# Kernel tuning notes

Measured on AMD Instinct MI355X. Metric: run time of the kernel, lower is better.

## Reference

```python
import math
import jax, jax.numpy as jnp
import numpy as np

N_HEADS = 8
FACTOR = 1.0


def setup_inputs() -> dict:
    key = jax.random.key(0)
    ks = jax.random.split(key, 5)
    B, L, D = 8, 4096, 512
    scale = 0.02
    def w(k):
        return jax.random.normal(k, (D, D), jnp.float32) * scale
    return {
        "hidden_states": jax.random.normal(ks[0], (B, L, D), jnp.float32),
        "Wq": w(ks[1]), "bq": jnp.zeros((D,), jnp.float32),
        "Wk": w(ks[2]), "bk": jnp.zeros((D,), jnp.float32),
        "Wv": w(ks[3]), "bv": jnp.zeros((D,), jnp.float32),
        "Wo": w(ks[4]), "bo": jnp.zeros((D,), jnp.float32),
    }


def reference(hidden_states, Wq, bq, Wk, bk, Wv, bv, Wo, bo):
    B, L, D = hidden_states.shape
    H = N_HEADS
    Hd = D // H

    def proj(W, b):
        y = hidden_states @ W.T + b                      # [B, L, D]
        return y.reshape(B, L, H, Hd).transpose(0, 2, 3, 1)  # [B, H, Hd, L]

    q = proj(Wq, bq)
    k = proj(Wk, bk)
    v = proj(Wv, bv)

    # period-based auto-correlation via FFT: corr(tau) = sum_t q(t) k(t - tau)
    qf = jnp.fft.rfft(q, axis=-1)
    kf = jnp.fft.rfft(k, axis=-1)
    corr = jnp.fft.irfft(qf * jnp.conj(kf), n=L, axis=-1)   # [B, H, Hd, L]

    # time-delay aggregation (eval branch): per-batch top-k delays
    mean_corr = corr.mean(axis=(1, 2))                      # [B, L]
    top_k = int(FACTOR * math.log(L))
    weights, delays = jax.lax.top_k(mean_corr, top_k)       # [B, k]
    weights = jax.nn.softmax(weights, axis=-1)

    # circular gather: pattern[b,h,d,i,l] = v[b,h,d,(l + delay[b,i]) % L]
    idx = (jnp.arange(L)[None, None, :] + delays[:, :, None]) % L  # [B, k, L]
    gathered = jax.vmap(lambda vb, ib: vb[:, :, ib])(v, idx)       # [B, H, Hd, k, L]
    agg = jnp.einsum("bhdkl,bk->bhdl", gathered, weights)          # [B, H, Hd, L]

    ctx = agg.transpose(0, 3, 1, 2).reshape(B, L, D)        # [B, L, D]
    return ctx @ Wo.T + bo
```

## Files before the change

kernel.cpp:

```cpp
#include <hip/hip_runtime.h>
#include <math.h>

#define NB 8
#define NL 4096
#define ND 512
#define NK 8

typedef unsigned short ushort_t;
typedef __bf16 bf16x8 __attribute__((ext_vector_type(8)));
typedef float f32x4 __attribute__((ext_vector_type(4)));

__device__ __forceinline__ unsigned short f2bf(float x) {
    unsigned u = __builtin_bit_cast(unsigned, x);
    u += 0x7fff + ((u >> 16) & 1);
    return (unsigned short)(u >> 16);
}
__device__ __forceinline__ float bf2f(unsigned short b) {
    unsigned u = ((unsigned)b) << 16;
    return __builtin_bit_cast(float, u);
}

__global__ void k_smallgemm(const float* __restrict__ A, const float* __restrict__ Bm,
                            float* __restrict__ C, int sa_k, int sa_i, int sb_k, int sb_j) {
    int i = blockIdx.y * 16 + threadIdx.y;
    int j = blockIdx.x * 16 + threadIdx.x;
    float acc = 0.f;
    for (int k = 0; k < ND; ++k)
        acc += A[k * sa_k + i * sa_i] * Bm[k * sb_k + j * sb_j];
    C[i * ND + j] = acc;
}

__global__ void k_biasprep(const float* __restrict__ Wo, const float* __restrict__ bv,
                           const float* __restrict__ bo, float* __restrict__ bp) {
    int i = blockIdx.x * blockDim.x + threadIdx.x;
    float acc = bo[i];
    for (int k = 0; k < ND; ++k) acc += Wo[i * ND + k] * bv[k];
    bp[i] = acc;
}

__global__ __launch_bounds__(256) void k_split(const float* __restrict__ src,
                                               ushort_t* __restrict__ dst) {
    int gid = blockIdx.x * 256 + threadIdx.x;
    int row = gid >> 7;
    int kc = (gid & 127) * 4;
    float4 v = *(const float4*)(src + (size_t)row * ND + kc);
    ushort4 hi, lo;
    hi.x = f2bf(v.x); lo.x = f2bf(v.x - bf2f(hi.x));
    hi.y = f2bf(v.y); lo.y = f2bf(v.y - bf2f(hi.y));
    hi.z = f2bf(v.z); lo.z = f2bf(v.z - bf2f(hi.z));
    hi.w = f2bf(v.w); lo.w = f2bf(v.w - bf2f(hi.w));
    *(ushort4*)(dst + (size_t)row * 1024 + kc) = hi;
    *(ushort4*)(dst + (size_t)row * 1024 + 512 + kc) = lo;
}

__global__ __launch_bounds__(256) void k_transpose(const float* __restrict__ X,
                                                   float* __restrict__ XT) {
    __shared__ float t[32][33];
    int b  = blockIdx.z;
    int l0 = blockIdx.x * 32;
    int c0 = blockIdx.y * 32;
    const float* Xb = X + (size_t)b * NL * ND;
    float* XTb = XT + (size_t)b * ND * NL;
    int tx = threadIdx.x, ty = threadIdx.y;
#pragma unroll
    for (int j = 0; j < 4; ++j)
        t[ty + j * 8][tx] = Xb[(size_t)(l0 + ty + j * 8) * ND + c0 + tx];
    __syncthreads();
#pragma unroll
    for (int j = 0; j < 4; ++j)
        XTb[(size_t)(c0 + ty + j * 8) * NL + l0 + tx] = t[tx][ty + j * 8];
}

template <int EPI>
__global__ __launch_bounds__(512, 2) void k_gemm_split(const ushort_t* __restrict__ As,
                                                       const ushort_t* __restrict__ Bs,
                                                       const float* __restrict__ bp,
                                                       float* __restrict__ Out) {
    struct Buf { ushort_t ahi[256 * 32]; ushort_t alo[256 * 32];
                 ushort_t bhi[256 * 32]; ushort_t blo[256 * 32]; };
    __shared__ union USm {
        Buf s[2];
        float t[32 * 257];
    } sm;
    const int tid = threadIdx.x;
    const int flat = blockIdx.x + (blockIdx.y << 7);
    const int wswz = ((flat & 7) << 5) + (flat >> 3);
    const int l0 = (wswz >> 1) * 256;
    const int n0 = (wswz & 1) * 256;
    const int lane = tid & 63;
    const int w = tid >> 6;
    const int wr = (w & 1) * 128;
    const int wc = (w >> 1) * 64;
    const int m = lane & 15;
    const int quad = lane >> 4;

    f32x4 acc[8][4];
#pragma unroll
    for (int i = 0; i < 8; ++i)
#pragma unroll
        for (int j = 0; j < 4; ++j) acc[i][j] = (f32x4){0.f, 0.f, 0.f, 0.f};

    auto STAGE = [&](int bf, int k0) {
#pragma unroll
        for (int v = 0; v < 2; ++v) {
            int q = v * 512 + tid;
            int row = ((q >> 6) << 4) | (q & 15);
            int kc = (q >> 4) & 3;
            const ushort_t* asrc = As + (size_t)(l0 + row) * 1024 + k0 + kc * 8;
            __builtin_amdgcn_global_load_lds(
                (const __attribute__((address_space(1))) unsigned int*)asrc,
                (__attribute__((address_space(3))) unsigned int*)&sm.s[bf].ahi[q * 8], 16, 0, 0);
            __builtin_amdgcn_global_load_lds(
                (const __attribute__((address_space(1))) unsigned int*)(asrc + 512),
                (__attribute__((address_space(3))) unsigned int*)&sm.s[bf].alo[q * 8], 16, 0, 0);
            const ushort_t* bsrc = Bs + (size_t)(n0 + row) * 1024 + k0 + kc * 8;
            __builtin_amdgcn_global_load_lds(
                (const __attribute__((address_space(1))) unsigned int*)bsrc,
                (__attribute__((address_space(3))) unsigned int*)&sm.s[bf].bhi[q * 8], 16, 0, 0);
            __builtin_amdgcn_global_load_lds(
                (const __attribute__((address_space(1))) unsigned int*)(bsrc + 512),
                (__attribute__((address_space(3))) unsigned int*)&sm.s[bf].blo[q * 8], 16, 0, 0);
        }
    };

    auto COMPUTE = [&](int bf) {
        bf16x8 ah[8], al[8];
#pragma unroll
        for (int i = 0; i < 8; ++i) {
            int off = ((wr >> 4) + i) * 512 + lane * 8;
            ah[i] = *(const bf16x8*)&sm.s[bf].ahi[off];
            al[i] = *(const bf16x8*)&sm.s[bf].alo[off];
        }
        __builtin_amdgcn_s_setprio(1);
#pragma unroll
        for (int j = 0; j < 4; ++j) {
            int off = ((wc >> 4) + j) * 512 + lane * 8;
            bf16x8 bh = *(const bf16x8*)&sm.s[bf].bhi[off];
            bf16x8 bl = *(const bf16x8*)&sm.s[bf].blo[off];
#pragma unroll
            for (int i = 0; i < 8; ++i) {
                acc[i][j] = __builtin_amdgcn_mfma_f32_16x16x32_bf16(ah[i], bh, acc[i][j], 0, 0, 0);
                acc[i][j] = __builtin_amdgcn_mfma_f32_16x16x32_bf16(ah[i], bl, acc[i][j], 0, 0, 0);
                acc[i][j] = __builtin_amdgcn_mfma_f32_16x16x32_bf16(al[i], bh, acc[i][j], 0, 0, 0);
            }
        }
        __builtin_amdgcn_s_setprio(0);
    };

    STAGE(0, 0);
    STAGE(1, 32);
    for (int t = 0; t < 15; ++t) {
        asm volatile("s_waitcnt vmcnt(8)" ::: "memory");
        __builtin_amdgcn_sched_barrier(0);
        __builtin_amdgcn_s_barrier();
        COMPUTE(t & 1);
        asm volatile("s_waitcnt lgkmcnt(0)" ::: "memory");
        __builtin_amdgcn_sched_barrier(0);
        __builtin_amdgcn_s_barrier();
        __builtin_amdgcn_sched_barrier(0);
        if (t < 14) STAGE(t & 1, (t + 2) * 32);
    }
    asm volatile("s_waitcnt vmcnt(0)" ::: "memory");
    __builtin_amdgcn_sched_barrier(0);
    __builtin_amdgcn_s_barrier();
    COMPUTE(1);

    if (EPI == 1) {
#pragma unroll
        for (int j = 0; j < 4; ++j) {
            int col = n0 + wc + 16 * j + m;
            float bv = bp[col];
#pragma unroll
            for (int i = 0; i < 8; ++i) {
                size_t rbase = (size_t)(l0 + wr + 16 * i + quad * 4) * ND + col;
#pragma unroll
                for (int r = 0; r < 4; ++r)
                    Out[rbase + (size_t)r * ND] = acc[i][j][r] + bv;
            }
        }
    } else {
#pragma unroll
        for (int c = 0; c < 8; ++c) {
            __syncthreads();
            if ((wc >> 6) == (c >> 1)) {
                int jb = (c & 1) * 2;
#pragma unroll
                for (int jj = 0; jj < 2; ++jj) {
                    int j = jb + jj;
                    int cl = 16 * jj + m;
#pragma unroll
                    for (int i = 0; i < 8; ++i)
#pragma unroll
                        for (int r = 0; r < 4; ++r)
                            sm.t[cl * 257 + wr + 16 * i + quad * 4 + r] = acc[i][j][r];
                }
            }
            __syncthreads();
#pragma unroll
            for (int it = 0; it < 16; ++it) {
                int idx = it * 512 + tid;
                int cl = idx >> 8;
                int row = idx & 255;
                int rg = l0 + row;
                Out[((size_t)((rg >> 12) * ND + n0 + c * 32 + cl)) * NL + (rg & 4095)] =
                    sm.t[cl * 257 + row];
            }
        }
    }
}

template <int DIR>
__device__ __forceinline__ void fft16(float2* v) {
    const float ct[8] = {1.f, 0.923879533f, 0.707106781f, 0.382683432f,
                         0.f, -0.382683432f, -0.707106781f, -0.923879533f};
    const float st[8] = {0.f, 0.382683432f, 0.707106781f, 0.923879533f,
                         1.f, 0.923879533f, 0.707106781f, 0.382683432f};
    const int br[16] = {0, 8, 4, 12, 2, 10, 6, 14, 1, 9, 5, 13, 3, 11, 7, 15};
    float2 a[16];
#pragma unroll
    for (int i = 0; i < 16; ++i) a[i] = v[br[i]];
#pragma unroll
    for (int s = 1; s <= 4; ++s) {
        const int L = 1 << s, h = L >> 1;
#pragma unroll
        for (int g = 0; g < 16; g += L)
#pragma unroll
            for (int p = 0; p < h; ++p) {
                int k = p << (4 - s);
                float wr = ct[k];
                float wi = (DIR > 0) ? -st[k] : st[k];
                int i1 = g + p, i2 = i1 + h;
                float tr = wr * a[i2].x - wi * a[i2].y;
                float ti = wr * a[i2].y + wi * a[i2].x;
                a[i2].x = a[i1].x - tr; a[i2].y = a[i1].y - ti;
                a[i1].x += tr;          a[i1].y += ti;
            }
    }
#pragma unroll
    for (int i = 0; i < 16; ++i) v[i] = a[i];
}

__device__ __forceinline__ float2 cmul(float2 a, float2 b) {
    return make_float2(a.x * b.x - a.y * b.y, a.x * b.y + a.y * b.x);
}
#define PADI(i) ((i) + ((i) >> 4))

__global__ __launch_bounds__(256) void k_fft_fwd(const float* __restrict__ XT,
                                                 const float* __restrict__ YT,
                                                 float2* __restrict__ partial) {
    __shared__ float2 data[4352];
    const int t = threadIdx.x;
    const int b = blockIdx.x >> 6;
    const int g = blockIdx.x & 63;

    float sv, cv;
    sincosf(-6.283185307179586f * (float)(t & 15) / 256.0f, &sv, &cv);
    const float2 w2 = make_float2(cv, sv);
    sincosf(-6.283185307179586f * (float)t / 4096.0f, &sv, &cv);
    const float2 w3 = make_float2(cv, sv);

    float2 acc[16];
#pragma unroll
    for (int r = 0; r < 16; ++r) acc[r] = make_float2(0.f, 0.f);

    for (int ch = 0; ch < 8; ++ch) {
        int c = g * 8 + ch;
        const float* xr = XT + ((size_t)b * ND + c) * NL;
        const float* yr = YT + ((size_t)b * ND + c) * NL;
        float2 v[16];
#pragma unroll
        for (int mm = 0; mm < 16; ++mm)
            v[mm] = make_float2(xr[t + 256 * mm], yr[t + 256 * mm]);
        fft16<1>(v);
        __syncthreads();
#pragma unroll
        for (int mm = 0; mm < 16; ++mm) data[PADI(16 * t + mm)] = v[mm];
        __syncthreads();
#pragma unroll
        for (int mm = 0; mm < 16; ++mm) v[mm] = data[PADI(t + 256 * mm)];
        {
            float2 wm = make_float2(1.f, 0.f);
#pragma unroll
            for (int mm = 1; mm < 16; ++mm) { wm = cmul(wm, w2); v[mm] = cmul(v[mm], wm); }
        }
        fft16<1>(v);
        __syncthreads();
        {
            int base = (t >> 4) * 256 + (t & 15);
#pragma unroll
            for (int mm = 0; mm < 16; ++mm) data[PADI(base + 16 * mm)] = v[mm];
        }
        __syncthreads();
#pragma unroll
        for (int mm = 0; mm < 16; ++mm) v[mm] = data[PADI(t + 256 * mm)];
        {
            float2 wm = make_float2(1.f, 0.f);
#pragma unroll
            for (int mm = 1; mm < 16; ++mm) { wm = cmul(wm, w3); v[mm] = cmul(v[mm], wm); }
        }
        fft16<1>(v);
        __syncthreads();
#pragma unroll
        for (int mm = 0; mm < 16; ++mm) data[PADI(t + 256 * mm)] = v[mm];
        __syncthreads();
#pragma unroll
        for (int mm = 0; mm < 16; ++mm) {
            int f = t + 256 * mm;
            float2 A = v[mm];
            float2 Bz = data[PADI((4096 - f) & 4095)];
            acc[mm].x += 0.5f * (A.x * Bz.y + A.y * Bz.x);
            acc[mm].y += 0.25f * ((A.x * A.x + A.y * A.y) - (Bz.x * Bz.x + Bz.y * Bz.y));
        }
    }
    float2* out = partial + ((size_t)b * 64 + g) * 4096;
#pragma unroll
    for (int mm = 0; mm < 16; ++mm) out[256 * mm + t] = acc[mm];
}

__global__ __launch_bounds__(256) void k_reduce(const float2* __restrict__ partial,
                                                float2* __restrict__ Cf) {
    int b = blockIdx.x >> 4;
    int f = (blockIdx.x & 15) * 256 + threadIdx.x;
    float2 s = make_float2(0.f, 0.f);
    for (int g = 0; g < 64; ++g) {
        float2 v = partial[((size_t)(b * 64 + g)) * 4096 + f];
        s.x += v.x; s.y += v.y;
    }
    Cf[(size_t)b * 4096 + f] = s;
}

__global__ __launch_bounds__(256) void k_ifft(const float2* __restrict__ Cf,
                                              float* __restrict__ mc) {
    __shared__ float2 data[4352];
    const int t = threadIdx.x;
    const int b = blockIdx.x;
    float sv, cv;
    sincosf(6.283185307179586f * (float)(t & 15) / 256.0f, &sv, &cv);
    const float2 w2 = make_float2(cv, sv);
    sincosf(6.283185307179586f * (float)t / 4096.0f, &sv, &cv);
    const float2 w3 = make_float2(cv, sv);

    float2 v[16];
#pragma unroll
    for (int mm = 0; mm < 16; ++mm) v[mm] = Cf[(size_t)b * 4096 + t + 256 * mm];
    fft16<-1>(v);
#pragma unroll
    for (int mm = 0; mm < 16; ++mm) data[PADI(16 * t + mm)] = v[mm];
    __syncthreads();
#pragma unroll
    for (int mm = 0; mm < 16; ++mm) v[mm] = data[PADI(t + 256 * mm)];
    {
        float2 wm = make_float2(1.f, 0.f);
#pragma unroll
        for (int mm = 1; mm < 16; ++mm) { wm = cmul(wm, w2); v[mm] = cmul(v[mm], wm); }
    }
    fft16<-1>(v);
    __syncthreads();
    {
        int base = (t >> 4) * 256 + (t & 15);
#pragma unroll
        for (int mm = 0; mm < 16; ++mm) data[PADI(base + 16 * mm)] = v[mm];
    }
    __syncthreads();
#pragma unroll
    for (int mm = 0; mm < 16; ++mm) v[mm] = data[PADI(t + 256 * mm)];
    {
        float2 wm = make_float2(1.f, 0.f);
#pragma unroll
        for (int mm = 1; mm < 16; ++mm) { wm = cmul(wm, w3); v[mm] = cmul(v[mm], wm); }
    }
    fft16<-1>(v);
    const float scale = 1.0f / (4096.0f * 512.0f);
#pragma unroll
    for (int mm = 0; mm < 16; ++mm)
        mc[(size_t)b * NL + t + 256 * mm] = v[mm].x * scale;
}

__global__ __launch_bounds__(256) void k_topk(const float* __restrict__ mc,
                                              float* __restrict__ wts,
                                              int* __restrict__ dly) {
    __shared__ float vals[4096];
    __shared__ float rv[256];
    __shared__ int ri[256];
    __shared__ float tv[NK];
    __shared__ int tix[NK];
    const int tid = threadIdx.x;
    const int b = blockIdx.x;
    for (int t = tid; t < 4096; t += 256) vals[t] = mc[(size_t)b * NL + t];
    __syncthreads();
    for (int it = 0; it < NK; ++it) {
        float bv = -3.0e38f;
        int bi = 0;
        for (int t = tid; t < 4096; t += 256) {
            float v = vals[t];
            if (v > bv) { bv = v; bi = t; }
        }
        rv[tid] = bv;
        ri[tid] = bi;
        __syncthreads();
        for (int off = 128; off > 0; off >>= 1) {
            if (tid < off) {
                if (rv[tid + off] > rv[tid]) {
                    rv[tid] = rv[tid + off];
                    ri[tid] = ri[tid + off];
                }
            }
            __syncthreads();
        }
        if (tid == 0) {
            tv[it] = rv[0];
            tix[it] = ri[0];
            vals[ri[0]] = -3.0e38f;
        }
        __syncthreads();
    }
    if (tid == 0) {
        float mx = tv[0];
        float e[NK], s = 0.f;
        for (int i = 0; i < NK; ++i) { e[i] = expf(tv[i] - mx); s += e[i]; }
        for (int i = 0; i < NK; ++i) {
            wts[b * NK + i] = e[i] / s;
            dly[b * NK + i] = tix[i];
        }
    }
}

__global__ __launch_bounds__(256) void k_gather(const float* __restrict__ X,
                                                const float* __restrict__ wts,
                                                const int* __restrict__ dly,
                                                ushort_t* __restrict__ Xaggs) {
    __shared__ float sw[NK];
    __shared__ int sd[NK];
    int gid = blockIdx.x * 256 + threadIdx.x;
    int b = gid >> 19;
    int rem = gid & 524287;
    int l = rem >> 7;
    int c4 = rem & 127;
    if (threadIdx.x < NK) {
        sw[threadIdx.x] = wts[b * NK + threadIdx.x];
        sd[threadIdx.x] = dly[b * NK + threadIdx.x];
    }
    __syncthreads();
    const float4* Xb = (const float4*)X + (size_t)b * 524288;
    float4 s = make_float4(0.f, 0.f, 0.f, 0.f);
#pragma unroll
    for (int i = 0; i < NK; ++i) {
        int ls = (l + sd[i]) & (NL - 1);
        float4 v = Xb[(size_t)ls * 128 + c4];
        float w = sw[i];
        s.x += w * v.x;
        s.y += w * v.y;
        s.z += w * v.z;
        s.w += w * v.w;
    }
    ushort4 hi, lo;
    hi.x = f2bf(s.x); lo.x = f2bf(s.x - bf2f(hi.x));
    hi.y = f2bf(s.y); lo.y = f2bf(s.y - bf2f(hi.y));
    hi.z = f2bf(s.z); lo.z = f2bf(s.z - bf2f(hi.z));
    hi.w = f2bf(s.w); lo.w = f2bf(s.w - bf2f(hi.w));
    ushort_t* rowp = Xaggs + (size_t)(b * NL + l) * 1024;
    *(ushort4*)(rowp + c4 * 4) = hi;
    *(ushort4*)(rowp + 512 + c4 * 4) = lo;
}

extern "C" void kernel_launch(void* const* d_in, const int* in_sizes, int n_in,
                              void* d_out, int out_size, void* d_ws, size_t ws_size,
                              hipStream_t stream) {
    (void)in_sizes; (void)n_in; (void)out_size; (void)ws_size;
    const float* X  = (const float*)d_in[0];
    const float* Wq = (const float*)d_in[1];
    const float* Wk = (const float*)d_in[3];
    const float* Wv = (const float*)d_in[5];
    const float* bv = (const float*)d_in[6];
    const float* Wo = (const float*)d_in[7];
    const float* bo = (const float*)d_in[8];
    float* Out = (float*)d_out;

    char* ws = (char*)d_ws;
    const size_t MB = 1024 * 1024;
    float*    M     = (float*)(ws + 0 * MB);
    float*    Wov   = (float*)(ws + 1 * MB);
    ushort_t* BsM   = (ushort_t*)(ws + 2 * MB);
    ushort_t* BsW   = (ushort_t*)(ws + 3 * MB);
    float*    bp    = (float*)(ws + 4 * MB);
    float*    mc    = (float*)(ws + 4 * MB + 0x10000);
    float*    wts   = (float*)(ws + 4 * MB + 0x40000);
    int*      dly   = (int*)(ws + 4 * MB + 0x41000);
    float2*   Cf    = (float2*)(ws + 4 * MB + 0x80000);
    float2*   partial = (float2*)(ws + 5 * MB);
    ushort_t* Xs    = (ushort_t*)(ws + 21 * MB);
    float*    XT    = (float*)(ws + 21 * MB);
    float*    YT    = (float*)(ws + 85 * MB);
    ushort_t* Xaggs = (ushort_t*)(ws + 85 * MB);

    k_smallgemm<<<dim3(32, 32), dim3(16, 16), 0, stream>>>(Wq, Wk, M, ND, 1, ND, 1);
    k_smallgemm<<<dim3(32, 32), dim3(16, 16), 0, stream>>>(Wo, Wv, Wov, 1, ND, ND, 1);
    k_biasprep<<<1, 512, 0, stream>>>(Wo, bv, bo, bp);
    k_split<<<256, 256, 0, stream>>>(M, BsM);
    k_split<<<256, 256, 0, stream>>>(Wov, BsW);

    k_split<<<16384, 256, 0, stream>>>(X, Xs);
    k_gemm_split<0><<<dim3(128, 2), 512, 0, stream>>>(Xs, BsM, nullptr, YT);

    k_transpose<<<dim3(128, 16, NB), dim3(32, 8), 0, stream>>>(X, XT);

    k_fft_fwd<<<512, 256, 0, stream>>>(XT, YT, partial);
    k_reduce<<<128, 256, 0, stream>>>(partial, Cf);
    k_ifft<<<NB, 256, 0, stream>>>(Cf, mc);

    k_topk<<<NB, 256, 0, stream>>>(mc, wts, dly);

    k_gather<<<16384, 256, 0, stream>>>(X, wts, dly, Xaggs);

    k_gemm_split<1><<<dim3(128, 2), 512, 0, stream>>>(Xaggs, BsW, bp, Out);
}
```

Before: 598.2 us.

## Swizzle GEMM LDS tile layout and fuse inverse FFT with top-k

The GEMM staging now stores A and B tiles row-major in LDS with an XOR swizzle on the 8-element column chunk, and the MFMA fragment reads use the matching swizzled offsets. The goal is fewer LDS bank conflicts and more contiguous global reads per row. Separately, the inverse FFT kernel now writes its mean-correlation output straight into shared memory and runs top-k and softmax in the same block. This drops one launch and a global round trip, at the cost of more shared memory per block.

```diff
diff --git a/kernel.cpp b/kernel.cpp
--- a/kernel.cpp
+++ b/kernel.cpp
@@ -104,16 +104,16 @@
 #pragma unroll
         for (int v = 0; v < 2; ++v) {
             int q = v * 512 + tid;
-            int row = ((q >> 6) << 4) | (q & 15);
-            int kc = (q >> 4) & 3;
-            const ushort_t* asrc = As + (size_t)(l0 + row) * 1024 + k0 + kc * 8;
+            int r = q >> 2;
+            int c = (q & 3) ^ ((r >> 1) & 3);
+            const ushort_t* asrc = As + (size_t)(l0 + r) * 1024 + k0 + c * 8;
             __builtin_amdgcn_global_load_lds(
                 (const __attribute__((address_space(1))) unsigned int*)asrc,
                 (__attribute__((address_space(3))) unsigned int*)&sm.s[bf].ahi[q * 8], 16, 0, 0);
             __builtin_amdgcn_global_load_lds(
                 (const __attribute__((address_space(1))) unsigned int*)(asrc + 512),
                 (__attribute__((address_space(3))) unsigned int*)&sm.s[bf].alo[q * 8], 16, 0, 0);
-            const ushort_t* bsrc = Bs + (size_t)(n0 + row) * 1024 + k0 + kc * 8;
+            const ushort_t* bsrc = Bs + (size_t)(n0 + r) * 1024 + k0 + c * 8;
             __builtin_amdgcn_global_load_lds(
                 (const __attribute__((address_space(1))) unsigned int*)bsrc,
                 (__attribute__((address_space(3))) unsigned int*)&sm.s[bf].bhi[q * 8], 16, 0, 0);
@@ -127,14 +127,16 @@
         bf16x8 ah[8], al[8];
 #pragma unroll
         for (int i = 0; i < 8; ++i) {
-            int off = ((wr >> 4) + i) * 512 + lane * 8;
+            int row = wr + 16 * i + m;
+            int off = row * 32 + ((quad ^ ((row >> 1) & 3)) * 8);
             ah[i] = *(const bf16x8*)&sm.s[bf].ahi[off];
             al[i] = *(const bf16x8*)&sm.s[bf].alo[off];
         }
         __builtin_amdgcn_s_setprio(1);
 #pragma unroll
         for (int j = 0; j < 4; ++j) {
-            int off = ((wc >> 4) + j) * 512 + lane * 8;
+            int row = wc + 16 * j + m;
+            int off = row * 32 + ((quad ^ ((row >> 1) & 3)) * 8);
             bf16x8 bh = *(const bf16x8*)&sm.s[bf].bhi[off];
             bf16x8 bl = *(const bf16x8*)&sm.s[bf].blo[off];
 #pragma unroll
@@ -329,9 +331,15 @@
     Cf[(size_t)b * 4096 + f] = s;
 }
 
-__global__ __launch_bounds__(256) void k_ifft(const float2* __restrict__ Cf,
-                                              float* __restrict__ mc) {
+__global__ __launch_bounds__(256) void k_ifft_topk(const float2* __restrict__ Cf,
+                                                   float* __restrict__ wts,
+                                                   int* __restrict__ dly) {
     __shared__ float2 data[4352];
+    __shared__ float vals[4096];
+    __shared__ float rv[256];
+    __shared__ int ri[256];
+    __shared__ float tv[NK];
+    __shared__ int tix[NK];
     const int t = threadIdx.x;
     const int b = blockIdx.x;
     float sv, cv;
@@ -373,48 +381,36 @@
     const float scale = 1.0f / (4096.0f * 512.0f);
 #pragma unroll
     for (int mm = 0; mm < 16; ++mm)
-        mc[(size_t)b * NL + t + 256 * mm] = v[mm].x * scale;
-}
-
-__global__ __launch_bounds__(256) void k_topk(const float* __restrict__ mc,
-                                              float* __restrict__ wts,
-                                              int* __restrict__ dly) {
-    __shared__ float vals[4096];
-    __shared__ float rv[256];
-    __shared__ int ri[256];
-    __shared__ float tv[NK];
-    __shared__ int tix[NK];
-    const int tid = threadIdx.x;
-    const int b = blockIdx.x;
-    for (int t = tid; t < 4096; t += 256) vals[t] = mc[(size_t)b * NL + t];
+        vals[t + 256 * mm] = v[mm].x * scale;
     __syncthreads();
+
     for (int it = 0; it < NK; ++it) {
         float bv = -3.0e38f;
         int bi = 0;
-        for (int t = tid; t < 4096; t += 256) {
-            float v = vals[t];
-            if (v > bv) { bv = v; bi = t; }
-        }
-        rv[tid] = bv;
-        ri[tid] = bi;
+        for (int tt = t; tt < 4096; tt += 256) {
+            float vv = vals[tt];
+            if (vv > bv) { bv = vv; bi = tt; }
+        }
+        rv[t] = bv;
+        ri[t] = bi;
         __syncthreads();
         for (int off = 128; off > 0; off >>= 1) {
-            if (tid < off) {
-                if (rv[tid + off] > rv[tid]) {
-                    rv[tid] = rv[tid + off];
-                    ri[tid] = ri[tid + off];
+            if (t < off) {
+                if (rv[t + off] > rv[t]) {
+                    rv[t] = rv[t + off];
+                    ri[t] = ri[t + off];
                 }
             }
             __syncthreads();
         }
-        if (tid == 0) {
+        if (t == 0) {
             tv[it] = rv[0];
             tix[it] = ri[0];
             vals[ri[0]] = -3.0e38f;
         }
         __syncthreads();
     }
-    if (tid == 0) {
+    if (t == 0) {
         float mx = tv[0];
         float e[NK], s = 0.f;
         for (int i = 0; i < NK; ++i) { e[i] = expf(tv[i] - mx); s += e[i]; }
@@ -483,7 +479,6 @@
     ushort_t* BsM   = (ushort_t*)(ws + 2 * MB);
     ushort_t* BsW   = (ushort_t*)(ws + 3 * MB);
     float*    bp    = (float*)(ws + 4 * MB);
-    float*    mc    = (float*)(ws + 4 * MB + 0x10000);
     float*    wts   = (float*)(ws + 4 * MB + 0x40000);
     int*      dly   = (int*)(ws + 4 * MB + 0x41000);
     float2*   Cf    = (float2*)(ws + 4 * MB + 0x80000);
@@ -506,9 +501,7 @@
 
     k_fft_fwd<<<512, 256, 0, stream>>>(XT, YT, partial);
     k_reduce<<<128, 256, 0, stream>>>(partial, Cf);
-    k_ifft<<<NB, 256, 0, stream>>>(Cf, mc);
-
-    k_topk<<<NB, 256, 0, stream>>>(mc, wts, dly);
+    k_ifft_topk<<<NB, 256, 0, stream>>>(Cf, wts, dly);
 
     k_gather<<<16384, 256, 0, stream>>>(X, wts, dly, Xaggs);
 
```

Measured after the change: 577.0 us. 1.04x faster.
